# Optimization experiments

Measured on AMD Instinct MI355X. Metric: run time of the kernel, lower is better.

The kernel has to match this reference:

```python
import jax, jax.numpy as jnp
import numpy as np

B = 100        # number of queries
N = 50000      # n_node
E = 600000     # n_edges
D = 128        # in_dim = out_dim (hidden_dim)
A = 64         # attn_dim
R = 200        # n_rel -> rela_embed has 2*R+1 = 401 rows


def setup_inputs() -> dict:
    key = jax.random.key(0)
    ks = jax.random.split(key, 14)
    q_sub = jax.random.randint(ks[0], (B,), 0, N)
    q_rel = jax.random.randint(ks[1], (B,), 0, 2 * R + 1)
    # edges: [E, 6]; col0=r_idx(<B), col2=rel(<2R+1), col4=sub(<N), col5=obj(<N); cols 1,3 unused
    c0 = jax.random.randint(ks[2], (E,), 0, B)
    c2 = jax.random.randint(ks[3], (E,), 0, 2 * R + 1)
    c4 = jax.random.randint(ks[4], (E,), 0, N)
    c5 = jax.random.randint(ks[5], (E,), 0, N)
    z = jnp.zeros((E,), dtype=jnp.int32)
    edges = jnp.stack([c0, z, c2, z, c4, c5], axis=1)
    hidden = jax.random.normal(ks[6], (N, D), dtype=jnp.float32)
    # learned parameters
    rela_embed = jax.random.normal(ks[7], (2 * R + 1, D), dtype=jnp.float32) * 0.02
    Ws = jax.random.normal(ks[8], (D, A), dtype=jnp.float32) * 0.05   # Ws_attn.weight^T
    Wr = jax.random.normal(ks[9], (D, A), dtype=jnp.float32) * 0.05   # Wr_attn.weight^T
    Wqr = jax.random.normal(ks[10], (D, A), dtype=jnp.float32) * 0.05 # Wqr_attn.weight^T
    bqr = jnp.zeros((A,), dtype=jnp.float32)
    wa = jax.random.normal(ks[11], (A, 1), dtype=jnp.float32) * 0.05  # w_alpha.weight^T
    ba = jnp.zeros((1,), dtype=jnp.float32)
    Wh = jax.random.normal(ks[12], (D, D), dtype=jnp.float32) * 0.05  # W_h.weight^T
    return {"q_sub": q_sub, "q_rel": q_rel, "hidden": hidden, "edges": edges,
            "n_node": N, "rela_embed": rela_embed, "Ws": Ws, "Wr": Wr,
            "Wqr": Wqr, "bqr": bqr, "wa": wa, "ba": ba, "Wh": Wh}


def reference(q_sub, q_rel, hidden, edges, n_node, rela_embed, Ws, Wr, Wqr, bqr, wa, ba, Wh):
    sub = edges[:, 4]
    rel = edges[:, 2]
    obj = edges[:, 5]
    r_idx = edges[:, 0]
    hs = hidden[sub]                       # [E, D] gather
    hr = rela_embed[rel]                   # [E, D] gather
    h_qr = rela_embed[q_rel][r_idx]        # [B, D] then gather -> [E, D]
    # attention score per edge
    pre = hs @ Ws + hr @ Wr + h_qr @ Wqr + bqr          # [E, A]
    alpha = jax.nn.sigmoid(jax.nn.relu(pre) @ wa + ba)   # [E, 1]
    message = alpha * (hs + hr)                          # [E, D]
    message_agg = jax.ops.segment_sum(message, obj, num_segments=n_node)  # [N, D]
    hidden_new = message_agg @ Wh                        # act = identity ('idd')
    return hidden_new
```

## Files before the change

### kernel.cpp

```cpp
#include <hip/hip_runtime.h>

#define DD 128
#define AA 64

static inline int idiv_up(int a, int b) { return (a + b - 1) / b; }

__device__ __forceinline__ unsigned short f2bf(float f) {
    unsigned u = __float_as_uint(f);
    u += 0x7fff + ((u >> 16) & 1);
    return (unsigned short)(u >> 16);
}
__device__ __forceinline__ float bf2f(unsigned short h) {
    return __uint_as_float(((unsigned)h) << 16);
}

__global__ __launch_bounds__(256)
void proj_all_kernel(const float* __restrict__ hidden,
                     const float* __restrict__ rela,
                     const int* __restrict__ q_rel,
                     const float* __restrict__ Ws,
                     const float* __restrict__ Wr,
                     const float* __restrict__ Wqr,
                     const float* __restrict__ bqr,
                     const float* __restrict__ Wh,
                     unsigned short* __restrict__ hsWs16,
                     float* __restrict__ hiddenWh,
                     float* __restrict__ hrWr,
                     float* __restrict__ relaWh,
                     float* __restrict__ hqrWqr,
                     int N, int NR, int B, int nA, int nB) {
    __shared__ float lht[128 * 64];
    __shared__ float wbuf[128 * 64];
    const int t = threadIdx.x;
    const int bid = blockIdx.x;
    int type, rbase, nrows;
    const float* src;
    if (bid < nA)           { type = 0; rbase = bid * 64;             nrows = N;  src = hidden; }
    else if (bid < nA + nB) { type = 1; rbase = (bid - nA) * 64;      nrows = NR; src = rela; }
    else                    { type = 2; rbase = (bid - nA - nB) * 64; nrows = B;  src = rela; }

    const int row = t & 63;
    const int d0 = (t >> 6) * 32;
    const int gr = rbase + row;
    const float* srow = nullptr;
    if (gr < nrows) {
        const int sr = (type == 2) ? q_rel[gr] : gr;
        srow = src + (long)sr * DD;
    }
    #pragma unroll
    for (int j = 0; j < 8; ++j) {
        float4 v = make_float4(0.f, 0.f, 0.f, 0.f);
        if (srow) v = *(const float4*)&srow[d0 + j * 4];
        lht[(d0 + j * 4 + 0) * 64 + row] = v.x;
        lht[(d0 + j * 4 + 1) * 64 + row] = v.y;
        lht[(d0 + j * 4 + 2) * 64 + row] = v.z;
        lht[(d0 + j * 4 + 3) * 64 + row] = v.w;
    }

    const int r0 = (t & 15) * 4;
    const int c0 = (t >> 4) * 4;
    const int nph = (type == 2) ? 1 : 3;

    for (int p = 0; p < nph; ++p) {
        const float* W;
        int ldw, off;
        if (p == 0) {
            W = (type == 0) ? Ws : (type == 1) ? Wr : Wqr;
            ldw = 64; off = 0;
        } else {
            W = Wh; ldw = 128; off = (p - 1) * 64;
        }
        #pragma unroll
        for (int k = 0; k < 8192; k += 1024) {
            const int f = k + t * 4;
            *(float4*)&wbuf[f] = *(const float4*)&W[(long)(f >> 6) * ldw + off + (f & 63)];
        }
        __syncthreads();

        float acc[4][4] = {};
        #pragma unroll 4
        for (int d = 0; d < 128; ++d) {
            const float4 hv = *(const float4*)&lht[d * 64 + r0];
            const float4 wv = *(const float4*)&wbuf[d * 64 + c0];
            acc[0][0] = fmaf(hv.x, wv.x, acc[0][0]);
            acc[0][1] = fmaf(hv.x, wv.y, acc[0][1]);
            acc[0][2] = fmaf(hv.x, wv.z, acc[0][2]);
            acc[0][3] = fmaf(hv.x, wv.w, acc[0][3]);
            acc[1][0] = fmaf(hv.y, wv.x, acc[1][0]);
            acc[1][1] = fmaf(hv.y, wv.y, acc[1][1]);
            acc[1][2] = fmaf(hv.y, wv.z, acc[1][2]);
            acc[1][3] = fmaf(hv.y, wv.w, acc[1][3]);
            acc[2][0] = fmaf(hv.z, wv.x, acc[2][0]);
            acc[2][1] = fmaf(hv.z, wv.y, acc[2][1]);
            acc[2][2] = fmaf(hv.z, wv.z, acc[2][2]);
            acc[2][3] = fmaf(hv.z, wv.w, acc[2][3]);
            acc[3][0] = fmaf(hv.w, wv.x, acc[3][0]);
            acc[3][1] = fmaf(hv.w, wv.y, acc[3][1]);
            acc[3][2] = fmaf(hv.w, wv.z, acc[3][2]);
            acc[3][3] = fmaf(hv.w, wv.w, acc[3][3]);
        }

        #pragma unroll
        for (int i = 0; i < 4; ++i) {
            const int orow = rbase + r0 + i;
            if (orow >= nrows) continue;
            if (type == 0) {
                if (p == 0) {
                    ushort4 o;
                    o.x = f2bf(acc[i][0]); o.y = f2bf(acc[i][1]);
                    o.z = f2bf(acc[i][2]); o.w = f2bf(acc[i][3]);
                    *(ushort4*)&hsWs16[(long)orow * 64 + c0] = o;
                } else {
                    *(float4*)&hiddenWh[(long)orow * 128 + off + c0] =
                        make_float4(acc[i][0], acc[i][1], acc[i][2], acc[i][3]);
                }
            } else if (type == 1) {
                if (p == 0) {
                    *(float4*)&hrWr[(long)orow * 64 + c0] =
                        make_float4(acc[i][0], acc[i][1], acc[i][2], acc[i][3]);
                } else {
                    *(float4*)&relaWh[(long)orow * 128 + off + c0] =
                        make_float4(acc[i][0], acc[i][1], acc[i][2], acc[i][3]);
                }
            } else {
                const float4 bq = *(const float4*)&bqr[c0];
                *(float4*)&hqrWqr[(long)orow * 64 + c0] =
                    make_float4(acc[i][0] + bq.x, acc[i][1] + bq.y,
                                acc[i][2] + bq.z, acc[i][3] + bq.w);
            }
        }
        __syncthreads();
    }
}

__global__ void hist_kernel(const int* __restrict__ edges, int* deg, int E) {
    const int e = blockIdx.x * blockDim.x + threadIdx.x;
    if (e < E) atomicAdd(&deg[edges[(long)e * 6 + 5]], 1);
}

__global__ void scan1_kernel(const int* __restrict__ in, int* __restrict__ out,
                             int* __restrict__ bsum, int n) {
    __shared__ int tsum[256];
    const int t = threadIdx.x;
    const int base = blockIdx.x * 1024 + t * 4;
    int v[4];
    int s = 0;
    #pragma unroll
    for (int j = 0; j < 4; ++j) {
        v[j] = (base + j < n) ? in[base + j] : 0;
        s += v[j];
    }
    tsum[t] = s;
    __syncthreads();
    for (int o = 1; o < 256; o <<= 1) {
        int x = (t >= o) ? tsum[t - o] : 0;
        __syncthreads();
        tsum[t] += x;
        __syncthreads();
    }
    int run = (t > 0) ? tsum[t - 1] : 0;
    if (t == 255 && bsum) bsum[blockIdx.x] = tsum[255];
    #pragma unroll
    for (int j = 0; j < 4; ++j) {
        if (base + j < n) out[base + j] = run;
        run += v[j];
    }
}

__global__ void scan_add_kernel(int* offs, int* cur, const int* __restrict__ bsumx, int n) {
    const int i = blockIdx.x * blockDim.x + threadIdx.x;
    if (i < n) {
        const int v = offs[i] + bsumx[i >> 10];
        offs[i] = v;
        cur[i] = v;
    }
}

__global__ void scatter_kernel(const int* __restrict__ edges, int* cur,
                               int2* __restrict__ recs, int E) {
    const int e = blockIdx.x * blockDim.x + threadIdx.x;
    if (e >= E) return;
    const int* ed = edges + (long)e * 6;
    const int pos = atomicAdd(&cur[ed[5]], 1);
    recs[pos] = make_int2(ed[4], ed[2] | (ed[0] << 16));
}

__global__ __launch_bounds__(256)
void gather_kernel(const int2* __restrict__ recs,
                   const int* __restrict__ offs,
                   const unsigned short* __restrict__ hsWs16,
                   const float* __restrict__ hrWr,
                   const float* __restrict__ hqrWqr,
                   const float* __restrict__ hiddenWh,
                   const float* __restrict__ relaWh,
                   const float* __restrict__ wa,
                   const float* __restrict__ ba,
                   float* __restrict__ out, int N, int E) {
    const int lane = threadIdx.x & 63;
    const int g = lane >> 4;
    const int l = lane & 15;
    const int v = (int)((blockIdx.x * blockDim.x + threadIdx.x) >> 6);
    if (v >= N) return;
    const float4 wav = *(const float4*)&wa[l * 4];
    const float bar = ba[0];
    const int start = offs[v];
    const int end = (v + 1 < N) ? offs[v + 1] : E;

    float4 acc0 = make_float4(0.f, 0.f, 0.f, 0.f);
    float4 acc1 = make_float4(0.f, 0.f, 0.f, 0.f);

    for (int base = start; base < end; base += 4) {
        const int k = base + g;
        const bool valid = (k < end);
        const int2 rec = valid ? recs[k] : make_int2(0, 0);
        const int sub  = rec.x;
        const int rel  = rec.y & 0xffff;
        const int ridx = rec.y >> 16;

        const ushort4 hw = *(const ushort4*)&hsWs16[(long)sub * AA + l * 4];
        const float4 b4 = *(const float4*)&hrWr[rel * AA + l * 4];
        const float4 c4 = *(const float4*)&hqrWqr[ridx * AA + l * 4];
        float s = fmaxf(bf2f(hw.x) + b4.x + c4.x, 0.f) * wav.x;
        s = fmaf(fmaxf(bf2f(hw.y) + b4.y + c4.y, 0.f), wav.y, s);
        s = fmaf(fmaxf(bf2f(hw.z) + b4.z + c4.z, 0.f), wav.z, s);
        s = fmaf(fmaxf(bf2f(hw.w) + b4.w + c4.w, 0.f), wav.w, s);
        s += __shfl_xor(s, 1);
        s += __shfl_xor(s, 2);
        s += __shfl_xor(s, 4);
        s += __shfl_xor(s, 8);
        float alpha = __builtin_amdgcn_rcpf(1.0f + __expf(-(s + bar)));
        if (!valid) alpha = 0.0f;

        const float4 h0 = *(const float4*)&hiddenWh[(long)sub * DD + l * 8];
        const float4 h1 = *(const float4*)&hiddenWh[(long)sub * DD + l * 8 + 4];
        const float4 r0 = *(const float4*)&relaWh[rel * DD + l * 8];
        const float4 r1 = *(const float4*)&relaWh[rel * DD + l * 8 + 4];
        acc0.x = fmaf(alpha, h0.x + r0.x, acc0.x);
        acc0.y = fmaf(alpha, h0.y + r0.y, acc0.y);
        acc0.z = fmaf(alpha, h0.z + r0.z, acc0.z);
        acc0.w = fmaf(alpha, h0.w + r0.w, acc0.w);
        acc1.x = fmaf(alpha, h1.x + r1.x, acc1.x);
        acc1.y = fmaf(alpha, h1.y + r1.y, acc1.y);
        acc1.z = fmaf(alpha, h1.z + r1.z, acc1.z);
        acc1.w = fmaf(alpha, h1.w + r1.w, acc1.w);
    }

    #pragma unroll
    for (int o = 16; o <= 32; o <<= 1) {
        acc0.x += __shfl_xor(acc0.x, o);
        acc0.y += __shfl_xor(acc0.y, o);
        acc0.z += __shfl_xor(acc0.z, o);
        acc0.w += __shfl_xor(acc0.w, o);
        acc1.x += __shfl_xor(acc1.x, o);
        acc1.y += __shfl_xor(acc1.y, o);
        acc1.z += __shfl_xor(acc1.z, o);
        acc1.w += __shfl_xor(acc1.w, o);
    }
    if (g == 0) {
        *(float4*)&out[(long)v * DD + l * 8]     = acc0;
        *(float4*)&out[(long)v * DD + l * 8 + 4] = acc1;
    }
}

extern "C" void kernel_launch(void* const* d_in, const int* in_sizes, int n_in,
                              void* d_out, int out_size, void* d_ws, size_t ws_size,
                              hipStream_t stream) {
    const int*   q_rel  = (const int*)d_in[1];
    const float* hidden = (const float*)d_in[2];
    const int*   edges  = (const int*)d_in[3];
    const float* rela   = (const float*)d_in[5];
    const float* Ws     = (const float*)d_in[6];
    const float* Wr     = (const float*)d_in[7];
    const float* Wqr    = (const float*)d_in[8];
    const float* bqr    = (const float*)d_in[9];
    const float* wa     = (const float*)d_in[10];
    const float* ba     = (const float*)d_in[11];
    const float* Wh     = (const float*)d_in[12];

    const int B  = in_sizes[1];
    const int N  = in_sizes[2] / DD;
    const int E  = in_sizes[3] / 6;
    const int NR = in_sizes[5] / DD;

    float* out = (float*)d_out;

    unsigned short* hsWs16 = (unsigned short*)d_ws;
    float* hiddenWh = (float*)(hsWs16 + (size_t)N * AA);
    float* hrWr     = hiddenWh + (size_t)N * DD;
    float* relaWh   = hrWr + (size_t)NR * AA;
    float* hqrWqr   = relaWh + (size_t)NR * DD;
    int*   deg      = (int*)(hqrWqr + (size_t)B * AA);
    int*   cur      = deg  + N;
    int*   offs     = cur  + N;
    int*   bsum     = offs + N;
    int*   bsumx    = bsum + 64;
    int2*  recs     = (int2*)(bsumx + 64);

    const int nA = idiv_up(N, 64);
    const int nB = idiv_up(NR, 64);
    const int nC = idiv_up(B, 64);
    const int nb = idiv_up(N, 1024);

    hipMemsetAsync(deg, 0, (size_t)N * sizeof(int), stream);
    proj_all_kernel<<<nA + nB + nC, 256, 0, stream>>>(
        hidden, rela, q_rel, Ws, Wr, Wqr, bqr, Wh,
        hsWs16, hiddenWh, hrWr, relaWh, hqrWqr, N, NR, B, nA, nB);
    hist_kernel<<<idiv_up(E, 256), 256, 0, stream>>>(edges, deg, E);
    scan1_kernel<<<nb, 256, 0, stream>>>(deg, offs, bsum, N);
    scan1_kernel<<<1, 256, 0, stream>>>(bsum, bsumx, nullptr, nb);
    scan_add_kernel<<<idiv_up(N, 256), 256, 0, stream>>>(offs, cur, bsumx, N);
    scatter_kernel<<<idiv_up(E, 256), 256, 0, stream>>>(edges, cur, recs, E);
    gather_kernel<<<idiv_up(N * 64, 256), 256, 0, stream>>>(
        recs, offs, hsWs16, hrWr, hqrWqr, hiddenWh, relaWh, wa, ba, out, N, E);
}
```

Before: 281.1 us.

## Fuse histogram into projection, single-block scan, interleave node rows, unroll gather

The degree histogram now runs inside the projection kernel on odd block indices, so one launch does both. The three-kernel scan is replaced by a single 1024-thread block scan. The bf16 attention projection and the W_h projection of each node are packed into one 160-float row so the gather touches one contiguous row per edge. The gather loop handles two edges per lane group per iteration to get more loads in flight, and the scatter reads edge fields as int2 vectors. The single-block scan serialises over N, and the interleaved blocks launch a wider grid that includes idle blocks.

```diff
diff --git a/kernel.cpp b/kernel.cpp
--- a/kernel.cpp
+++ b/kernel.cpp
@@ -2,6 +2,7 @@
 
 #define DD 128
 #define AA 64
+#define SS 160
 
 static inline int idiv_up(int a, int b) { return (a + b - 1) / b; }
 
@@ -15,29 +16,46 @@
 }
 
 __global__ __launch_bounds__(256)
-void proj_all_kernel(const float* __restrict__ hidden,
-                     const float* __restrict__ rela,
-                     const int* __restrict__ q_rel,
-                     const float* __restrict__ Ws,
-                     const float* __restrict__ Wr,
-                     const float* __restrict__ Wqr,
-                     const float* __restrict__ bqr,
-                     const float* __restrict__ Wh,
-                     unsigned short* __restrict__ hsWs16,
-                     float* __restrict__ hiddenWh,
-                     float* __restrict__ hrWr,
-                     float* __restrict__ relaWh,
-                     float* __restrict__ hqrWqr,
-                     int N, int NR, int B, int nA, int nB) {
+void proj_hist_kernel(const float* __restrict__ hidden,
+                      const float* __restrict__ rela,
+                      const int* __restrict__ q_rel,
+                      const float* __restrict__ Ws,
+                      const float* __restrict__ Wr,
+                      const float* __restrict__ Wqr,
+                      const float* __restrict__ bqr,
+                      const float* __restrict__ Wh,
+                      const int* __restrict__ edges,
+                      int* __restrict__ deg,
+                      float* __restrict__ subrows,
+                      float* __restrict__ hrWr,
+                      float* __restrict__ relaWh,
+                      float* __restrict__ hqrWqr,
+                      int N, int NR, int B, int E,
+                      int nA, int nB, int nC, int nH) {
     __shared__ float lht[128 * 64];
     __shared__ float wbuf[128 * 64];
     const int t = threadIdx.x;
     const int bid = blockIdx.x;
+
+    if (bid & 1) {
+        const int hb = bid >> 1;
+        if (hb >= nH) return;
+        const int ebase = hb * 1024;
+        #pragma unroll
+        for (int j = 0; j < 4; ++j) {
+            const int e = ebase + j * 256 + t;
+            if (e < E) atomicAdd(&deg[edges[(long)e * 6 + 5]], 1);
+        }
+        return;
+    }
+
+    const int pb = bid >> 1;
+    if (pb >= nA + nB + nC) return;
     int type, rbase, nrows;
     const float* src;
-    if (bid < nA)           { type = 0; rbase = bid * 64;             nrows = N;  src = hidden; }
-    else if (bid < nA + nB) { type = 1; rbase = (bid - nA) * 64;      nrows = NR; src = rela; }
-    else                    { type = 2; rbase = (bid - nA - nB) * 64; nrows = B;  src = rela; }
+    if (pb < nA)           { type = 0; rbase = pb * 64;             nrows = N;  src = hidden; }
+    else if (pb < nA + nB) { type = 1; rbase = (pb - nA) * 64;      nrows = NR; src = rela; }
+    else                   { type = 2; rbase = (pb - nA - nB) * 64; nrows = B;  src = rela; }
 
     const int row = t & 63;
     const int d0 = (t >> 6) * 32;
@@ -105,13 +123,14 @@
             const int orow = rbase + r0 + i;
             if (orow >= nrows) continue;
             if (type == 0) {
+                float* srw = subrows + (long)orow * SS;
                 if (p == 0) {
                     ushort4 o;
                     o.x = f2bf(acc[i][0]); o.y = f2bf(acc[i][1]);
                     o.z = f2bf(acc[i][2]); o.w = f2bf(acc[i][3]);
-                    *(ushort4*)&hsWs16[(long)orow * 64 + c0] = o;
+                    *(ushort4*)((unsigned short*)srw + c0) = o;
                 } else {
-                    *(float4*)&hiddenWh[(long)orow * 128 + off + c0] =
+                    *(float4*)(srw + 32 + off + c0) =
                         make_float4(acc[i][0], acc[i][1], acc[i][2], acc[i][3]);
                 }
             } else if (type == 1) {
@@ -133,46 +152,49 @@
     }
 }
 
-__global__ void hist_kernel(const int* __restrict__ edges, int* deg, int E) {
-    const int e = blockIdx.x * blockDim.x + threadIdx.x;
-    if (e < E) atomicAdd(&deg[edges[(long)e * 6 + 5]], 1);
-}
-
-__global__ void scan1_kernel(const int* __restrict__ in, int* __restrict__ out,
-                             int* __restrict__ bsum, int n) {
-    __shared__ int tsum[256];
+__global__ __launch_bounds__(1024)
+void scan_kernel(const int* __restrict__ deg, int* __restrict__ offs,
+                 int* __restrict__ cur, int N) {
+    __shared__ int wsum[17];
     const int t = threadIdx.x;
-    const int base = blockIdx.x * 1024 + t * 4;
-    int v[4];
-    int s = 0;
-    #pragma unroll
-    for (int j = 0; j < 4; ++j) {
-        v[j] = (base + j < n) ? in[base + j] : 0;
-        s += v[j];
-    }
-    tsum[t] = s;
-    __syncthreads();
-    for (int o = 1; o < 256; o <<= 1) {
-        int x = (t >= o) ? tsum[t - o] : 0;
-        __syncthreads();
-        tsum[t] += x;
-        __syncthreads();
-    }
-    int run = (t > 0) ? tsum[t - 1] : 0;
-    if (t == 255 && bsum) bsum[blockIdx.x] = tsum[255];
-    #pragma unroll
-    for (int j = 0; j < 4; ++j) {
-        if (base + j < n) out[base + j] = run;
-        run += v[j];
-    }
-}
-
-__global__ void scan_add_kernel(int* offs, int* cur, const int* __restrict__ bsumx, int n) {
-    const int i = blockIdx.x * blockDim.x + threadIdx.x;
-    if (i < n) {
-        const int v = offs[i] + bsumx[i >> 10];
-        offs[i] = v;
-        cur[i] = v;
+    const int lane = t & 63;
+    const int wv = t >> 6;
+    int carry = 0;
+    for (int base = 0; base < N; base += 4096) {
+        const int i0 = base + t * 4;
+        int v0 = 0, v1 = 0, v2 = 0, v3 = 0;
+        if (i0 + 3 < N) {
+            const int4 q = *(const int4*)&deg[i0];
+            v0 = q.x; v1 = q.y; v2 = q.z; v3 = q.w;
+        } else {
+            if (i0 + 0 < N) v0 = deg[i0 + 0];
+            if (i0 + 1 < N) v1 = deg[i0 + 1];
+            if (i0 + 2 < N) v2 = deg[i0 + 2];
+            if (i0 + 3 < N) v3 = deg[i0 + 3];
+        }
+        const int s = v0 + v1 + v2 + v3;
+        int inc = s;
+        #pragma unroll
+        for (int o = 1; o < 64; o <<= 1) {
+            const int x = __shfl_up(inc, o, 64);
+            if (lane >= o) inc += x;
+        }
+        if (lane == 63) wsum[wv] = inc;
+        __syncthreads();
+        if (t == 0) {
+            int run = 0;
+            #pragma unroll
+            for (int k = 0; k < 16; ++k) { const int tmp = wsum[k]; wsum[k] = run; run += tmp; }
+            wsum[16] = run;
+        }
+        __syncthreads();
+        int e = carry + wsum[wv] + (inc - s);
+        if (i0 + 0 < N) { offs[i0 + 0] = e; cur[i0 + 0] = e; } e += v0;
+        if (i0 + 1 < N) { offs[i0 + 1] = e; cur[i0 + 1] = e; } e += v1;
+        if (i0 + 2 < N) { offs[i0 + 2] = e; cur[i0 + 2] = e; } e += v2;
+        if (i0 + 3 < N) { offs[i0 + 3] = e; cur[i0 + 3] = e; } e += v3;
+        carry += wsum[16];
+        __syncthreads();
     }
 }
 
@@ -180,18 +202,19 @@
                                int2* __restrict__ recs, int E) {
     const int e = blockIdx.x * blockDim.x + threadIdx.x;
     if (e >= E) return;
-    const int* ed = edges + (long)e * 6;
-    const int pos = atomicAdd(&cur[ed[5]], 1);
-    recs[pos] = make_int2(ed[4], ed[2] | (ed[0] << 16));
+    const int2 a = *(const int2*)&edges[(long)e * 6];
+    const int2 b = *(const int2*)&edges[(long)e * 6 + 2];
+    const int2 c = *(const int2*)&edges[(long)e * 6 + 4];
+    const int pos = atomicAdd(&cur[c.y], 1);
+    recs[pos] = make_int2(c.x, b.x | (a.x << 16));
 }
 
 __global__ __launch_bounds__(256)
 void gather_kernel(const int2* __restrict__ recs,
                    const int* __restrict__ offs,
-                   const unsigned short* __restrict__ hsWs16,
+                   const float* __restrict__ subrows,
                    const float* __restrict__ hrWr,
                    const float* __restrict__ hqrWqr,
-                   const float* __restrict__ hiddenWh,
                    const float* __restrict__ relaWh,
                    const float* __restrict__ wa,
                    const float* __restrict__ ba,
@@ -209,40 +232,66 @@
     float4 acc0 = make_float4(0.f, 0.f, 0.f, 0.f);
     float4 acc1 = make_float4(0.f, 0.f, 0.f, 0.f);
 
-    for (int base = start; base < end; base += 4) {
-        const int k = base + g;
-        const bool valid = (k < end);
-        const int2 rec = valid ? recs[k] : make_int2(0, 0);
-        const int sub  = rec.x;
-        const int rel  = rec.y & 0xffff;
-        const int ridx = rec.y >> 16;
-
-        const ushort4 hw = *(const ushort4*)&hsWs16[(long)sub * AA + l * 4];
-        const float4 b4 = *(const float4*)&hrWr[rel * AA + l * 4];
-        const float4 c4 = *(const float4*)&hqrWqr[ridx * AA + l * 4];
-        float s = fmaxf(bf2f(hw.x) + b4.x + c4.x, 0.f) * wav.x;
-        s = fmaf(fmaxf(bf2f(hw.y) + b4.y + c4.y, 0.f), wav.y, s);
-        s = fmaf(fmaxf(bf2f(hw.z) + b4.z + c4.z, 0.f), wav.z, s);
-        s = fmaf(fmaxf(bf2f(hw.w) + b4.w + c4.w, 0.f), wav.w, s);
-        s += __shfl_xor(s, 1);
-        s += __shfl_xor(s, 2);
-        s += __shfl_xor(s, 4);
-        s += __shfl_xor(s, 8);
-        float alpha = __builtin_amdgcn_rcpf(1.0f + __expf(-(s + bar)));
-        if (!valid) alpha = 0.0f;
-
-        const float4 h0 = *(const float4*)&hiddenWh[(long)sub * DD + l * 8];
-        const float4 h1 = *(const float4*)&hiddenWh[(long)sub * DD + l * 8 + 4];
-        const float4 r0 = *(const float4*)&relaWh[rel * DD + l * 8];
-        const float4 r1 = *(const float4*)&relaWh[rel * DD + l * 8 + 4];
-        acc0.x = fmaf(alpha, h0.x + r0.x, acc0.x);
-        acc0.y = fmaf(alpha, h0.y + r0.y, acc0.y);
-        acc0.z = fmaf(alpha, h0.z + r0.z, acc0.z);
-        acc0.w = fmaf(alpha, h0.w + r0.w, acc0.w);
-        acc1.x = fmaf(alpha, h1.x + r1.x, acc1.x);
-        acc1.y = fmaf(alpha, h1.y + r1.y, acc1.y);
-        acc1.z = fmaf(alpha, h1.z + r1.z, acc1.z);
-        acc1.w = fmaf(alpha, h1.w + r1.w, acc1.w);
+    for (int base = start; base < end; base += 8) {
+        const int k1 = base + g;
+        const int k2 = base + 4 + g;
+        const bool va1 = (k1 < end);
+        const bool va2 = (k2 < end);
+        const int2 rc1 = va1 ? recs[k1] : make_int2(0, 0);
+        const int2 rc2 = va2 ? recs[k2] : make_int2(0, 0);
+        const int sub1 = rc1.x, rel1 = rc1.y & 0xffff, rid1 = rc1.y >> 16;
+        const int sub2 = rc2.x, rel2 = rc2.y & 0xffff, rid2 = rc2.y >> 16;
+        const float* sr1 = subrows + (long)sub1 * SS;
+        const float* sr2 = subrows + (long)sub2 * SS;
+
+        const ushort4 hw1 = *(const ushort4*)((const unsigned short*)sr1 + l * 4);
+        const ushort4 hw2 = *(const ushort4*)((const unsigned short*)sr2 + l * 4);
+        const float4 b41 = *(const float4*)&hrWr[rel1 * AA + l * 4];
+        const float4 b42 = *(const float4*)&hrWr[rel2 * AA + l * 4];
+        const float4 c41 = *(const float4*)&hqrWqr[rid1 * AA + l * 4];
+        const float4 c42 = *(const float4*)&hqrWqr[rid2 * AA + l * 4];
+        const float4 h01 = *(const float4*)(sr1 + 32 + l * 8);
+        const float4 h11 = *(const float4*)(sr1 + 32 + l * 8 + 4);
+        const float4 h02 = *(const float4*)(sr2 + 32 + l * 8);
+        const float4 h12 = *(const float4*)(sr2 + 32 + l * 8 + 4);
+        const float4 r01 = *(const float4*)&relaWh[rel1 * DD + l * 8];
+        const float4 r11 = *(const float4*)&relaWh[rel1 * DD + l * 8 + 4];
+        const float4 r02 = *(const float4*)&relaWh[rel2 * DD + l * 8];
+        const float4 r12 = *(const float4*)&relaWh[rel2 * DD + l * 8 + 4];
+
+        float s1 = fmaxf(bf2f(hw1.x) + b41.x + c41.x, 0.f) * wav.x;
+        s1 = fmaf(fmaxf(bf2f(hw1.y) + b41.y + c41.y, 0.f), wav.y, s1);
+        s1 = fmaf(fmaxf(bf2f(hw1.z) + b41.z + c41.z, 0.f), wav.z, s1);
+        s1 = fmaf(fmaxf(bf2f(hw1.w) + b41.w + c41.w, 0.f), wav.w, s1);
+        float s2 = fmaxf(bf2f(hw2.x) + b42.x + c42.x, 0.f) * wav.x;
+        s2 = fmaf(fmaxf(bf2f(hw2.y) + b42.y + c42.y, 0.f), wav.y, s2);
+        s2 = fmaf(fmaxf(bf2f(hw2.z) + b42.z + c42.z, 0.f), wav.z, s2);
+        s2 = fmaf(fmaxf(bf2f(hw2.w) + b42.w + c42.w, 0.f), wav.w, s2);
+        s1 += __shfl_xor(s1, 1);  s2 += __shfl_xor(s2, 1);
+        s1 += __shfl_xor(s1, 2);  s2 += __shfl_xor(s2, 2);
+        s1 += __shfl_xor(s1, 4);  s2 += __shfl_xor(s2, 4);
+        s1 += __shfl_xor(s1, 8);  s2 += __shfl_xor(s2, 8);
+        float al1 = __builtin_amdgcn_rcpf(1.0f + __expf(-(s1 + bar)));
+        float al2 = __builtin_amdgcn_rcpf(1.0f + __expf(-(s2 + bar)));
+        if (!va1) al1 = 0.0f;
+        if (!va2) al2 = 0.0f;
+
+        acc0.x = fmaf(al1, h01.x + r01.x, acc0.x);
+        acc0.y = fmaf(al1, h01.y + r01.y, acc0.y);
+        acc0.z = fmaf(al1, h01.z + r01.z, acc0.z);
+        acc0.w = fmaf(al1, h01.w + r01.w, acc0.w);
+        acc1.x = fmaf(al1, h11.x + r11.x, acc1.x);
+        acc1.y = fmaf(al1, h11.y + r11.y, acc1.y);
+        acc1.z = fmaf(al1, h11.z + r11.z, acc1.z);
+        acc1.w = fmaf(al1, h11.w + r11.w, acc1.w);
+        acc0.x = fmaf(al2, h02.x + r02.x, acc0.x);
+        acc0.y = fmaf(al2, h02.y + r02.y, acc0.y);
+        acc0.z = fmaf(al2, h02.z + r02.z, acc0.z);
+        acc0.w = fmaf(al2, h02.w + r02.w, acc0.w);
+        acc1.x = fmaf(al2, h12.x + r12.x, acc1.x);
+        acc1.y = fmaf(al2, h12.y + r12.y, acc1.y);
+        acc1.z = fmaf(al2, h12.z + r12.z, acc1.z);
+        acc1.w = fmaf(al2, h12.w + r12.w, acc1.w);
     }
 
     #pragma unroll
@@ -284,32 +333,28 @@
 
     float* out = (float*)d_out;
 
-    unsigned short* hsWs16 = (unsigned short*)d_ws;
-    float* hiddenWh = (float*)(hsWs16 + (size_t)N * AA);
-    float* hrWr     = hiddenWh + (size_t)N * DD;
-    float* relaWh   = hrWr + (size_t)NR * AA;
-    float* hqrWqr   = relaWh + (size_t)NR * DD;
-    int*   deg      = (int*)(hqrWqr + (size_t)B * AA);
-    int*   cur      = deg  + N;
-    int*   offs     = cur  + N;
-    int*   bsum     = offs + N;
-    int*   bsumx    = bsum + 64;
-    int2*  recs     = (int2*)(bsumx + 64);
+    float* subrows = (float*)d_ws;
+    float* hrWr    = subrows + (size_t)N * SS;
+    float* relaWh  = hrWr + (size_t)NR * AA;
+    float* hqrWqr  = relaWh + (size_t)NR * DD;
+    int*   deg     = (int*)(hqrWqr + (size_t)B * AA);
+    int*   cur     = deg  + N;
+    int*   offs    = cur  + N;
+    int2*  recs    = (int2*)(offs + N);
 
     const int nA = idiv_up(N, 64);
     const int nB = idiv_up(NR, 64);
     const int nC = idiv_up(B, 64);
-    const int nb = idiv_up(N, 1024);
+    const int nH = idiv_up(E, 1024);
+    const int nP = nA + nB + nC;
+    const int grid_ph = 2 * ((nP > nH) ? nP : nH);
 
     hipMemsetAsync(deg, 0, (size_t)N * sizeof(int), stream);
-    proj_all_kernel<<<nA + nB + nC, 256, 0, stream>>>(
-        hidden, rela, q_rel, Ws, Wr, Wqr, bqr, Wh,
-        hsWs16, hiddenWh, hrWr, relaWh, hqrWqr, N, NR, B, nA, nB);
-    hist_kernel<<<idiv_up(E, 256), 256, 0, stream>>>(edges, deg, E);
-    scan1_kernel<<<nb, 256, 0, stream>>>(deg, offs, bsum, N);
-    scan1_kernel<<<1, 256, 0, stream>>>(bsum, bsumx, nullptr, nb);
-    scan_add_kernel<<<idiv_up(N, 256), 256, 0, stream>>>(offs, cur, bsumx, N);
+    proj_hist_kernel<<<grid_ph, 256, 0, stream>>>(
+        hidden, rela, q_rel, Ws, Wr, Wqr, bqr, Wh, edges, deg,
+        subrows, hrWr, relaWh, hqrWqr, N, NR, B, E, nA, nB, nC, nH);
+    scan_kernel<<<1, 1024, 0, stream>>>(deg, offs, cur, N);
     scatter_kernel<<<idiv_up(E, 256), 256, 0, stream>>>(edges, cur, recs, E);
     gather_kernel<<<idiv_up(N * 64, 256), 256, 0, stream>>>(
-        recs, offs, hsWs16, hrWr, hqrWqr, hiddenWh, relaWh, wa, ba, out, N, E);
-}
+        recs, offs, subrows, hrWr, hqrWqr, relaWh, wa, ba, out, N, E);
+}
```

Measured after the change: 320.5 us. 1.14x slower.
